# Kernel optimization log

Hardware: AMD Instinct MI355X
Metric: run time of the kernel (lower is better)

Reference implementation:

```python
import jax, jax.numpy as jnp
import numpy as np


def _edt(mask):
    """Exact Euclidean distance transform of a binary [H,W] mask.

    Matches scipy.ndimage.distance_transform_edt: for nonzero pixels,
    distance to the nearest zero pixel (0 at zero pixels).
    Two-pass exact algorithm: 1D distance along rows (axis 0) per column,
    then D[i,j] = min_k d1[i,k]^2 + (j-k)^2 (Felzenszwalb-Huttenlocher identity).
    """
    H, W = mask.shape
    BIG = jnp.float32(H + W)  # larger than any real pixel distance
    zero = mask == 0
    idx = jnp.arange(H, dtype=jnp.float32)[:, None]  # [H,1]
    # nearest zero above (inclusive)
    up = jax.lax.cummax(jnp.where(zero, idx, -BIG), axis=0)
    d_up = idx - up
    # nearest zero below (inclusive): cummin from the bottom
    dn = -jnp.flip(jax.lax.cummax(jnp.flip(jnp.where(zero, -idx, -2 * BIG), axis=0), axis=0), axis=0)
    d_dn = dn - idx
    d1 = jnp.minimum(jnp.minimum(d_up, d_dn), BIG)  # [H,W] 1D column distance
    d1sq = d1 * d1
    j = jnp.arange(W, dtype=jnp.float32)
    off = (j[:, None] - j[None, :]) ** 2  # [W,W], off[j,k]
    # D[i,j] = min_k d1sq[i,k] + (j-k)^2
    Dsq = jnp.min(d1sq[:, None, :] + off[None, :, :], axis=-1)  # [H,W]
    return jnp.sqrt(Dsq)


def _phi_level_set(mask):
    """Normalized signed distance map for one [H,W] binary mask."""
    dist_inside = _edt(mask)
    dist_outside = _edt(1.0 - mask)
    phi = dist_outside - dist_inside
    denom = jnp.max(jnp.abs(phi)) + 1e-8
    return jnp.where(jnp.any(mask > 0), phi / denom, jnp.zeros_like(phi))


def _combined_loss(predictions, targets):
    probs = jax.nn.sigmoid(predictions)
    # Dice
    p = probs.reshape(-1)
    t = targets.reshape(-1)
    smooth = 1e-6
    inter = jnp.sum(p * t)
    dice = 1.0 - (2.0 * inter + smooth) / (jnp.sum(p) + jnp.sum(t) + smooth)
    # Boundary: phi is computed from detached targets (constant)
    masks = jax.lax.stop_gradient(targets)[:, 0]  # [B,H,W]
    phi = jax.vmap(_phi_level_set)(masks)[:, None]  # [B,1,H,W]
    boundary = jnp.mean(phi * probs)
    # BCE with logits (numerically stable)
    x = predictions
    bce = jnp.mean(jnp.clip(x, 0.0, None) - x * targets + jnp.log1p(jnp.exp(-jnp.abs(x))))
    # rebalance schedule at epoch 0: alpha = initial_alpha = 0.005
    alpha = 0.005
    beta = max(0.0, 0.6 - alpha)
    return (1.0 - beta) * dice + beta * boundary + 0.4 * bce


def setup_inputs() -> dict:
    key = jax.random.key(0)
    k1, k2 = jax.random.split(key)
    B, C, H, W = 16, 1, 256, 256
    predictions = jax.random.normal(k1, (B, C, H, W), dtype=jnp.float32)
    targets = (jax.random.uniform(k2, (B, C, H, W)) < 0.3).astype(jnp.float32)
    return {"predictions": predictions, "targets": targets}


def reference(predictions, targets):
    return _combined_loss(predictions, targets)
```

## Files before the change

kernel.cpp:

```cpp
#include <hip/hip_runtime.h>
#include <math.h>

#define BB 16
#define HH 256
#define WW 256
#define NPIX (BB*HH*WW)
#define CH 16
#define RPC 16
#define ROWS 8
#define NRB (BB*HH/ROWS)
#define PADW 4
#define GSTRIDE (WW + 2*PADW)


__global__ __launch_bounds__(64) void zbuild_kernel(const float4* __restrict__ targ4,
                                                    ushort4* __restrict__ zb4) {
    int blk = blockIdx.x;
    int t = threadIdx.x;
    const float4* m = targ4 + (size_t)blk * RPC * (WW / 4) + t;
    unsigned z0 = 0, z1 = 0, z2 = 0, z3 = 0;
    #pragma unroll
    for (int r = 0; r < RPC; ++r) {
        float4 v = m[r * (WW / 4)];
        if (v.x == 0.0f) z0 |= 1u << r;
        if (v.y == 0.0f) z1 |= 1u << r;
        if (v.z == 0.0f) z2 |= 1u << r;
        if (v.w == 0.0f) z3 |= 1u << r;
    }
    ushort4 o;
    o.x = (unsigned short)z0; o.y = (unsigned short)z1;
    o.z = (unsigned short)z2; o.w = (unsigned short)z3;
    zb4[blk * (WW / 4) + t] = o;
}

__global__ __launch_bounds__(256) void rowmin_fused_kernel(const unsigned short* __restrict__ zb,
                                                           const float* __restrict__ pred,
                                                           float* __restrict__ partials) {
    int g = blockIdx.x;
    int b = g >> 5;
    int r0 = (g & 31) << 3;
    int C = r0 >> 4;
    int rb0 = r0 & 15;
    int j = threadIdx.x;

    int la0 = -1, la1 = -1;
    int fb0 = 100000, fb1 = 100000;
    unsigned zoc = 0;
    #pragma unroll
    for (int c = 0; c < CH; ++c) {
        unsigned z = (unsigned)zb[((b * CH + c) << 8) + j];
        unsigned zi = (~z) & 0xFFFFu;
        if (c < C) {
            if (z)  la0 = (c << 4) + (31 - __clz(z));
            if (zi) la1 = (c << 4) + (31 - __clz(zi));
        } else if (c > C) {
            if (z  && fb0 == 100000) fb0 = (c << 4) + (__ffs(z) - 1);
            if (zi && fb1 == 100000) fb1 = (c << 4) + (__ffs(zi) - 1);
        } else {
            zoc = z;
        }
    }
    unsigned zoc1 = (~zoc) & 0xFFFFu;

    float x[ROWS];
    #pragma unroll
    for (int r = 0; r < ROWS; ++r)
        x[r] = pred[(((b << 8) + (r0 + r)) << 8) + j];

    __shared__ float gg[ROWS][2][GSTRIDE];
    if (j < 2 * ROWS * 2 * PADW) {
        int r = j >> 4, f = (j >> 3) & 1, p = j & 7;
        gg[r][f][(p < PADW) ? p : (WW + p)] = 1e30f;
    }

    #pragma unroll
    for (int r = 0; r < ROWS; ++r) {
        int rb = rb0 + r;
        int i = r0 + r;
        unsigned below = zoc & ((2u << rb) - 1u);
        int lz = below ? ((C << 4) + (31 - __clz(below))) : la0;
        unsigned above = zoc & (0xFFFFu & ~((1u << rb) - 1u));
        int fz = above ? ((C << 4) + (__ffs(above) - 1)) : fb0;
        int da = (lz < 0) ? 100000 : (i - lz);
        int d0 = min(min(da, fz - i), 512);
        float f0 = (float)d0;
        gg[r][0][PADW + j] = f0 * f0;
        unsigned below1 = zoc1 & ((2u << rb) - 1u);
        int lz1 = below1 ? ((C << 4) + (31 - __clz(below1))) : la1;
        unsigned above1 = zoc1 & (0xFFFFu & ~((1u << rb) - 1u));
        int fz1 = above1 ? ((C << 4) + (__ffs(above1) - 1)) : fb1;
        int da1 = (lz1 < 0) ? 100000 : (i - lz1);
        int d1v = min(min(da1, fz1 - i), 512);
        float f1 = (float)d1v;
        gg[r][1][PADW + j] = f1 * f1;
    }
    __syncthreads();

    float sp = 0.f, st = 0.f, spt = 0.f, sbce = 0.f, sphip = 0.f, amax = 0.f;
    #pragma unroll
    for (int r = 0; r < ROWS; ++r) {
        int rb = rb0 + r;
        bool msk = (((zoc >> rb) & 1u) == 0u);
        const float* bsel = &gg[r][msk ? 0 : 1][0];
        float best = 1e30f;
        #pragma unroll
        for (int c = 0; c <= 2 * PADW; ++c) {
            float Cc = (float)((PADW - c) * (PADW - c));
            best = fminf(best, bsel[j + c] + Cc);
        }
        if (__any(best > 25.0f)) {
            const float* bs = bsel + PADW;
            for (int k = 0; k < WW; ++k) {
                float df = (float)(j - k);
                best = fminf(best, bs[k] + df * df);
            }
        }
        float dd = sqrtf(best);
        float phi = msk ? -dd : dd;
        float xr = x[r];
        float ax = fabsf(xr);
        float q = __expf(-ax);
        float pa = 1.0f / (1.0f + q);
        float p = (xr >= 0.0f) ? pa : q * pa;
        sp += p;
        st += msk ? 1.0f : 0.0f;
        spt += msk ? p : 0.0f;
        sbce += fmaxf(xr, 0.0f) - (msk ? xr : 0.0f) - __logf(pa);
        sphip += phi * p;
        amax = fmaxf(amax, fabsf(phi));
    }

    #pragma unroll
    for (int off = 32; off > 0; off >>= 1) {
        sp    += __shfl_down(sp,    off, 64);
        st    += __shfl_down(st,    off, 64);
        spt   += __shfl_down(spt,   off, 64);
        sbce  += __shfl_down(sbce,  off, 64);
        sphip += __shfl_down(sphip, off, 64);
        amax   = fmaxf(amax,  __shfl_down(amax,  off, 64));
    }
    __shared__ float red[4][8];
    int lane = j & 63, wv = j >> 6;
    if (lane == 0) {
        red[wv][0] = sp; red[wv][1] = st; red[wv][2] = spt; red[wv][3] = sbce;
        red[wv][4] = sphip; red[wv][5] = amax;
    }
    __syncthreads();
    if (j == 0) {
        float* o = partials + g * 8;
        #pragma unroll
        for (int q2 = 0; q2 < 5; ++q2)
            o[q2] = red[0][q2] + red[1][q2] + red[2][q2] + red[3][q2];
        o[5] = fmaxf(fmaxf(red[0][5], red[1][5]), fmaxf(red[2][5], red[3][5]));
    }
}

__global__ __launch_bounds__(256) void final_kernel(const float* __restrict__ partials,
                                                    float* __restrict__ out) {
    int t = threadIdx.x;
    float s0 = 0.f, s1 = 0.f, s2 = 0.f, s3 = 0.f, s4 = 0.f, m5 = 0.f;
    #pragma unroll
    for (int e = 0; e < 2; ++e) {
        const float* rec = partials + ((t * 2 + e) << 3);
        s0 += rec[0]; s1 += rec[1]; s2 += rec[2]; s3 += rec[3];
        s4 += rec[4];
        m5 = fmaxf(m5, rec[5]);
    }
    __shared__ float arr[256][3];
    arr[t][0] = s4; arr[t][1] = m5; arr[t][2] = s1;
    __syncthreads();
    __shared__ float bnd[16];
    if (t < 16) {
        float Sb = 0.f, Mb = 0.f, STb = 0.f;
        for (int e = 0; e < 16; ++e) {
            Sb += arr[t * 16 + e][0];
            Mb = fmaxf(Mb, arr[t * 16 + e][1]);
            STb += arr[t * 16 + e][2];
        }
        bnd[t] = (STb > 0.0f) ? (Sb / (Mb + 1e-8f)) : 0.0f;
    }
    #pragma unroll
    for (int off = 32; off > 0; off >>= 1) {
        s0 += __shfl_down(s0, off, 64);
        s1 += __shfl_down(s1, off, 64);
        s2 += __shfl_down(s2, off, 64);
        s3 += __shfl_down(s3, off, 64);
    }
    __shared__ float wred[4][4];
    int lane = t & 63, wv = t >> 6;
    if (lane == 0) { wred[wv][0] = s0; wred[wv][1] = s1; wred[wv][2] = s2; wred[wv][3] = s3; }
    __syncthreads();
    if (t == 0) {
        float sp   = wred[0][0] + wred[1][0] + wred[2][0] + wred[3][0];
        float st   = wred[0][1] + wred[1][1] + wred[2][1] + wred[3][1];
        float spt  = wred[0][2] + wred[1][2] + wred[2][2] + wred[3][2];
        float sbce = wred[0][3] + wred[1][3] + wred[2][3] + wred[3][3];
        float sbnd = 0.f;
        #pragma unroll
        for (int bb2 = 0; bb2 < BB; ++bb2) sbnd += bnd[bb2];
        float dice = 1.0f - (2.0f * spt + 1e-6f) / (sp + st + 1e-6f);
        float invN = 1.0f / (float)NPIX;
        float boundary = sbnd * invN;
        float bce = sbce * invN;
        float alpha = 0.005f;
        float beta = 0.6f - alpha;
        out[0] = (1.0f - beta) * dice + beta * boundary + 0.4f * bce;
    }
}

extern "C" void kernel_launch(void* const* d_in, const int* in_sizes, int n_in,
                              void* d_out, int out_size, void* d_ws, size_t ws_size,
                              hipStream_t stream) {
    (void)in_sizes; (void)n_in; (void)out_size; (void)ws_size;
    const float* pred = (const float*)d_in[0];
    const float* targ = (const float*)d_in[1];
    unsigned short* zb = (unsigned short*)d_ws;
    float* partials = (float*)((char*)d_ws + BB * CH * WW * sizeof(unsigned short));

    zbuild_kernel<<<BB * CH, 64, 0, stream>>>((const float4*)targ, (ushort4*)zb);
    rowmin_fused_kernel<<<NRB, 256, 0, stream>>>(zb, pred, partials);
    final_kernel<<<1, 256, 0, stream>>>(partials, (float*)d_out);
}
```

Before: 71.72 us.

## Fuse zero-bitmask build and final reduction into single kernel with last-block atomic

Drops the separate bitmask-build and final-reduction kernels. Each block now builds its image's column zero-bitmasks in shared memory by reading the whole 256x256 target image, and the last block to finish, found with an atomic counter, performs the final reduction. This removes two launches and the global bitmask round trip, at the cost of every one of the 32 blocks per image re-reading the full target image. It also adds a memset per call.

```diff
diff --git a/kernel.cpp b/kernel.cpp
--- a/kernel.cpp
+++ b/kernel.cpp
@@ -13,29 +13,11 @@
 #define GSTRIDE (WW + 2*PADW)
 
 
-__global__ __launch_bounds__(64) void zbuild_kernel(const float4* __restrict__ targ4,
-                                                    ushort4* __restrict__ zb4) {
-    int blk = blockIdx.x;
-    int t = threadIdx.x;
-    const float4* m = targ4 + (size_t)blk * RPC * (WW / 4) + t;
-    unsigned z0 = 0, z1 = 0, z2 = 0, z3 = 0;
-    #pragma unroll
-    for (int r = 0; r < RPC; ++r) {
-        float4 v = m[r * (WW / 4)];
-        if (v.x == 0.0f) z0 |= 1u << r;
-        if (v.y == 0.0f) z1 |= 1u << r;
-        if (v.z == 0.0f) z2 |= 1u << r;
-        if (v.w == 0.0f) z3 |= 1u << r;
-    }
-    ushort4 o;
-    o.x = (unsigned short)z0; o.y = (unsigned short)z1;
-    o.z = (unsigned short)z2; o.w = (unsigned short)z3;
-    zb4[blk * (WW / 4) + t] = o;
-}
-
-__global__ __launch_bounds__(256) void rowmin_fused_kernel(const unsigned short* __restrict__ zb,
-                                                           const float* __restrict__ pred,
-                                                           float* __restrict__ partials) {
+__global__ __launch_bounds__(256) void fused_kernel(const float* __restrict__ pred,
+                                                    const float4* __restrict__ targ4,
+                                                    float* __restrict__ partials,
+                                                    unsigned* __restrict__ flag,
+                                                    float* __restrict__ out) {
     int g = blockIdx.x;
     int b = g >> 5;
     int r0 = (g & 31) << 3;
@@ -43,12 +25,46 @@
     int rb0 = r0 & 15;
     int j = threadIdx.x;
 
+    __shared__ unsigned short zbS[CH][WW];
+    __shared__ float gg[ROWS][2][GSTRIDE];
+    __shared__ float red[4][8];
+    __shared__ float arrF[256][3];
+    __shared__ float bnd[BB];
+    __shared__ float wred[4][4];
+    __shared__ unsigned lastBlk;
+
+    const float4* img = targ4 + (size_t)b * HH * (WW / 4);
+    #pragma unroll
+    for (int k = 0; k < 4; ++k) {
+        int T = (k << 8) + j;
+        int c = T >> 6, q = T & 63;
+        const float4* m = img + (c * RPC) * (WW / 4) + q;
+        unsigned z0 = 0, z1 = 0, z2 = 0, z3 = 0;
+        #pragma unroll
+        for (int r = 0; r < RPC; ++r) {
+            float4 v = m[r * (WW / 4)];
+            if (v.x == 0.0f) z0 |= 1u << r;
+            if (v.y == 0.0f) z1 |= 1u << r;
+            if (v.z == 0.0f) z2 |= 1u << r;
+            if (v.w == 0.0f) z3 |= 1u << r;
+        }
+        ushort4 o;
+        o.x = (unsigned short)z0; o.y = (unsigned short)z1;
+        o.z = (unsigned short)z2; o.w = (unsigned short)z3;
+        *reinterpret_cast<ushort4*>(&zbS[c][q << 2]) = o;
+    }
+    if (j < 2 * ROWS * 2 * PADW) {
+        int r = j >> 4, f = (j >> 3) & 1, p = j & 7;
+        gg[r][f][(p < PADW) ? p : (WW + p)] = 1e30f;
+    }
+    __syncthreads();
+
     int la0 = -1, la1 = -1;
     int fb0 = 100000, fb1 = 100000;
     unsigned zoc = 0;
     #pragma unroll
     for (int c = 0; c < CH; ++c) {
-        unsigned z = (unsigned)zb[((b * CH + c) << 8) + j];
+        unsigned z = (unsigned)zbS[c][j];
         unsigned zi = (~z) & 0xFFFFu;
         if (c < C) {
             if (z)  la0 = (c << 4) + (31 - __clz(z));
@@ -66,12 +82,6 @@
     #pragma unroll
     for (int r = 0; r < ROWS; ++r)
         x[r] = pred[(((b << 8) + (r0 + r)) << 8) + j];
-
-    __shared__ float gg[ROWS][2][GSTRIDE];
-    if (j < 2 * ROWS * 2 * PADW) {
-        int r = j >> 4, f = (j >> 3) & 1, p = j & 7;
-        gg[r][f][(p < PADW) ? p : (WW + p)] = 1e30f;
-    }
 
     #pragma unroll
     for (int r = 0; r < ROWS; ++r) {
@@ -139,72 +149,72 @@
         sphip += __shfl_down(sphip, off, 64);
         amax   = fmaxf(amax,  __shfl_down(amax,  off, 64));
     }
-    __shared__ float red[4][8];
     int lane = j & 63, wv = j >> 6;
     if (lane == 0) {
         red[wv][0] = sp; red[wv][1] = st; red[wv][2] = spt; red[wv][3] = sbce;
         red[wv][4] = sphip; red[wv][5] = amax;
     }
     __syncthreads();
+
     if (j == 0) {
-        float* o = partials + g * 8;
+        float* o = partials + (g << 3);
         #pragma unroll
         for (int q2 = 0; q2 < 5; ++q2)
             o[q2] = red[0][q2] + red[1][q2] + red[2][q2] + red[3][q2];
         o[5] = fmaxf(fmaxf(red[0][5], red[1][5]), fmaxf(red[2][5], red[3][5]));
-    }
-}
-
-__global__ __launch_bounds__(256) void final_kernel(const float* __restrict__ partials,
-                                                    float* __restrict__ out) {
-    int t = threadIdx.x;
-    float s0 = 0.f, s1 = 0.f, s2 = 0.f, s3 = 0.f, s4 = 0.f, m5 = 0.f;
-    #pragma unroll
-    for (int e = 0; e < 2; ++e) {
-        const float* rec = partials + ((t * 2 + e) << 3);
-        s0 += rec[0]; s1 += rec[1]; s2 += rec[2]; s3 += rec[3];
-        s4 += rec[4];
-        m5 = fmaxf(m5, rec[5]);
-    }
-    __shared__ float arr[256][3];
-    arr[t][0] = s4; arr[t][1] = m5; arr[t][2] = s1;
-    __syncthreads();
-    __shared__ float bnd[16];
-    if (t < 16) {
-        float Sb = 0.f, Mb = 0.f, STb = 0.f;
-        for (int e = 0; e < 16; ++e) {
-            Sb += arr[t * 16 + e][0];
-            Mb = fmaxf(Mb, arr[t * 16 + e][1]);
-            STb += arr[t * 16 + e][2];
-        }
-        bnd[t] = (STb > 0.0f) ? (Sb / (Mb + 1e-8f)) : 0.0f;
-    }
-    #pragma unroll
-    for (int off = 32; off > 0; off >>= 1) {
-        s0 += __shfl_down(s0, off, 64);
-        s1 += __shfl_down(s1, off, 64);
-        s2 += __shfl_down(s2, off, 64);
-        s3 += __shfl_down(s3, off, 64);
-    }
-    __shared__ float wred[4][4];
-    int lane = t & 63, wv = t >> 6;
-    if (lane == 0) { wred[wv][0] = s0; wred[wv][1] = s1; wred[wv][2] = s2; wred[wv][3] = s3; }
-    __syncthreads();
-    if (t == 0) {
-        float sp   = wred[0][0] + wred[1][0] + wred[2][0] + wred[3][0];
-        float st   = wred[0][1] + wred[1][1] + wred[2][1] + wred[3][1];
-        float spt  = wred[0][2] + wred[1][2] + wred[2][2] + wred[3][2];
-        float sbce = wred[0][3] + wred[1][3] + wred[2][3] + wred[3][3];
-        float sbnd = 0.f;
-        #pragma unroll
-        for (int bb2 = 0; bb2 < BB; ++bb2) sbnd += bnd[bb2];
-        float dice = 1.0f - (2.0f * spt + 1e-6f) / (sp + st + 1e-6f);
-        float invN = 1.0f / (float)NPIX;
-        float boundary = sbnd * invN;
-        float bce = sbce * invN;
-        float alpha = 0.005f;
-        float beta = 0.6f - alpha;
-        out[0] = (1.0f - beta) * dice + beta * boundary + 0.4f * bce;
+        __builtin_amdgcn_fence(__ATOMIC_RELEASE, "agent");
+        unsigned prev = atomicAdd(flag, 1u);
+        lastBlk = (prev == (unsigned)(NRB - 1)) ? 1u : 0u;
+    }
+    __syncthreads();
+    if (lastBlk) {
+        __builtin_amdgcn_fence(__ATOMIC_ACQUIRE, "agent");
+        int t = j;
+        float s0 = 0.f, s1 = 0.f, s2 = 0.f, s3 = 0.f, s4 = 0.f, m5 = 0.f;
+        #pragma unroll
+        for (int e = 0; e < 2; ++e) {
+            const float* rec = partials + (((t << 1) + e) << 3);
+            s0 += rec[0]; s1 += rec[1]; s2 += rec[2]; s3 += rec[3];
+            s4 += rec[4];
+            m5 = fmaxf(m5, rec[5]);
+        }
+        arrF[t][0] = s4; arrF[t][1] = m5; arrF[t][2] = s1;
+        __syncthreads();
+        if (t < 16) {
+            float Sb = 0.f, Mb = 0.f, STb = 0.f;
+            for (int e = 0; e < 16; ++e) {
+                Sb += arrF[t * 16 + e][0];
+                Mb = fmaxf(Mb, arrF[t * 16 + e][1]);
+                STb += arrF[t * 16 + e][2];
+            }
+            bnd[t] = (STb > 0.0f) ? (Sb / (Mb + 1e-8f)) : 0.0f;
+        }
+        #pragma unroll
+        for (int off = 32; off > 0; off >>= 1) {
+            s0 += __shfl_down(s0, off, 64);
+            s1 += __shfl_down(s1, off, 64);
+            s2 += __shfl_down(s2, off, 64);
+            s3 += __shfl_down(s3, off, 64);
+        }
+        int lane2 = t & 63, wv2 = t >> 6;
+        if (lane2 == 0) { wred[wv2][0] = s0; wred[wv2][1] = s1; wred[wv2][2] = s2; wred[wv2][3] = s3; }
+        __syncthreads();
+        if (t == 0) {
+            float sp2   = wred[0][0] + wred[1][0] + wred[2][0] + wred[3][0];
+            float st2   = wred[0][1] + wred[1][1] + wred[2][1] + wred[3][1];
+            float spt2  = wred[0][2] + wred[1][2] + wred[2][2] + wred[3][2];
+            float sbce2 = wred[0][3] + wred[1][3] + wred[2][3] + wred[3][3];
+            float sbnd = 0.f;
+            #pragma unroll
+            for (int bb2 = 0; bb2 < BB; ++bb2) sbnd += bnd[bb2];
+            float dice = 1.0f - (2.0f * spt2 + 1e-6f) / (sp2 + st2 + 1e-6f);
+            float invN = 1.0f / (float)NPIX;
+            float boundary = sbnd * invN;
+            float bce = sbce2 * invN;
+            float alpha = 0.005f;
+            float beta = 0.6f - alpha;
+            out[0] = (1.0f - beta) * dice + beta * boundary + 0.4f * bce;
+        }
     }
 }
 
@@ -214,10 +224,9 @@
     (void)in_sizes; (void)n_in; (void)out_size; (void)ws_size;
     const float* pred = (const float*)d_in[0];
     const float* targ = (const float*)d_in[1];
-    unsigned short* zb = (unsigned short*)d_ws;
-    float* partials = (float*)((char*)d_ws + BB * CH * WW * sizeof(unsigned short));
-
-    zbuild_kernel<<<BB * CH, 64, 0, stream>>>((const float4*)targ, (ushort4*)zb);
-    rowmin_fused_kernel<<<NRB, 256, 0, stream>>>(zb, pred, partials);
-    final_kernel<<<1, 256, 0, stream>>>(partials, (float*)d_out);
+    float* partials = (float*)d_ws;
+    unsigned* flag = (unsigned*)((char*)d_ws + NRB * 8 * sizeof(float));
+
+    hipMemsetAsync(flag, 0, sizeof(unsigned), stream);
+    fused_kernel<<<NRB, 256, 0, stream>>>(pred, (const float4*)targ, partials, flag, (float*)d_out);
 }
```

Result: slower. 79.16 us (+10.4%).
